# Performance work log

Hardware: AMD Instinct MI355X
Metric: run time of the kernel (lower is better)

## Reference

```python
import jax, jax.numpy as jnp
import numpy as np

N_EMBD = 1024
N_HEAD = 16
MASK_FILL = -10000.0


def setup_inputs() -> dict:
    key = jax.random.key(0)
    ks = jax.random.split(key, 9)
    s = 1.0 / np.sqrt(N_EMBD)
    d = {"x": jax.random.normal(ks[0], (4, 2048, N_EMBD), dtype=jnp.float32)}
    for i, name in enumerate(["k", "q", "v", "p"]):
        d[f"W{name}"] = jax.random.uniform(ks[1 + 2 * i], (N_EMBD, N_EMBD), minval=-s, maxval=s, dtype=jnp.float32)
        d[f"b{name}"] = jax.random.uniform(ks[2 + 2 * i], (N_EMBD,), minval=-s, maxval=s, dtype=jnp.float32)
    return d


def reference(x, Wk, bk, Wq, bq, Wv, bv, Wp, bp):
    B, T, C = x.shape
    H, D = N_HEAD, C // N_HEAD
    # projections -> [B, H, T, D]
    def split_heads(y):
        return y.reshape(B, T, H, D).transpose(0, 2, 1, 3)
    k = split_heads(x @ Wk + bk)
    q = split_heads(x @ Wq + bq)
    v = split_heads(x @ Wv + bv)
    att = jnp.einsum("bhtd,bhsd->bhts", q, k) / jnp.sqrt(jnp.float32(D))
    causal = jnp.tril(jnp.ones((T, T), dtype=bool))  # [T, T]
    att = jnp.where(causal[None, None], att, MASK_FILL)
    att = jax.nn.softmax(att, axis=-1)
    y = jnp.einsum("bhts,bhsd->bhtd", att, v)
    y = y.transpose(0, 2, 1, 3).reshape(B, T, C)
    return y @ Wp + bp
```

## Files before the change

### kernel.cpp

```cpp
#include <hip/hip_runtime.h>
#include <hip/hip_bf16.h>

#define CDIM   1024
#define NHEADS 16
#define DHEAD  64
#define BATCH  4
#define TSEQ   2048
#define MROWS  (BATCH * TSEQ)
#define QSTR   3072
#define NEG_BIG (-1e30f)
#define MASKVAL (-3.0e38f)
#define SCALE_L2E 0.18033688011f
#define DEFER_TH 11.5416f

typedef __attribute__((ext_vector_type(8)))  short bf16x8;
typedef __attribute__((ext_vector_type(4)))  float f32x4;
typedef __attribute__((ext_vector_type(16))) float f32x16;

__device__ __forceinline__ unsigned short f2bf(float f) {
    __hip_bfloat16 h = __float2bfloat16(f);
    return *reinterpret_cast<unsigned short*>(&h);
}
__device__ __forceinline__ unsigned int cvtpk(float a, float b) {
    unsigned r;
    asm("v_cvt_pk_bf16_f32 %0, %1, %2" : "=v"(r) : "v"(a), "v"(b));
    return r;
}
__device__ __forceinline__ float ex2(float x) {
    float r; asm("v_exp_f32 %0, %1" : "=v"(r) : "v"(x)); return r;
}

__global__ __launch_bounds__(256)
void cvt_x_kernel(const float* __restrict__ in, unsigned short* __restrict__ out)
{
    size_t i = (size_t)blockIdx.x * 256 + threadIdx.x;
    const float4* p = reinterpret_cast<const float4*>(in) + i * 2;
    float4 a = p[0], b = p[1];
    uint4 o;
    o.x = (unsigned)f2bf(a.x) | ((unsigned)f2bf(a.y) << 16);
    o.y = (unsigned)f2bf(a.z) | ((unsigned)f2bf(a.w) << 16);
    o.z = (unsigned)f2bf(b.x) | ((unsigned)f2bf(b.y) << 16);
    o.w = (unsigned)f2bf(b.z) | ((unsigned)f2bf(b.w) << 16);
    *reinterpret_cast<uint4*>(out + i * 8) = o;
}

__global__ __launch_bounds__(256)
void wt_kernel(const float* __restrict__ W0, const float* __restrict__ W1,
               const float* __restrict__ W2, const float* __restrict__ W3,
               unsigned short* __restrict__ T0, unsigned short* __restrict__ T1,
               unsigned short* __restrict__ T2, unsigned short* __restrict__ T3)
{
    const float* W; unsigned short* T;
    switch (blockIdx.z) {
        case 0:  W = W0; T = T0; break;
        case 1:  W = W1; T = T1; break;
        case 2:  W = W2; T = T2; break;
        default: W = W3; T = T3; break;
    }
    __shared__ float tile[32][33];
    const int t = threadIdx.x;
    const int r = t >> 3;
    const int c4 = (t & 7) * 4;
    const int n0 = blockIdx.x * 32, k0 = blockIdx.y * 32;
    float4 v = *reinterpret_cast<const float4*>(&W[(size_t)(k0 + r) * CDIM + n0 + c4]);
    tile[r][c4 + 0] = v.x; tile[r][c4 + 1] = v.y;
    tile[r][c4 + 2] = v.z; tile[r][c4 + 3] = v.w;
    __syncthreads();
    uint2 o;
    o.x = (unsigned)f2bf(tile[c4 + 0][r]) | ((unsigned)f2bf(tile[c4 + 1][r]) << 16);
    o.y = (unsigned)f2bf(tile[c4 + 2][r]) | ((unsigned)f2bf(tile[c4 + 3][r]) << 16);
    *reinterpret_cast<uint2*>(&T[(size_t)(n0 + r) * CDIM + k0 + c4]) = o;
}

__global__ __launch_bounds__(256)
void pack_bias(const float* __restrict__ bq, const float* __restrict__ bk,
               const float* __restrict__ bv, float* __restrict__ o)
{
    int i = blockIdx.x * 256 + threadIdx.x;
    float v = (i < 1024) ? bq[i] : (i < 2048 ? bk[i - 1024] : bv[i - 2048]);
    o[i] = v;
}


#define GBAR8  asm volatile("s_barrier" ::: "memory")
#define LGKM0  asm volatile("s_waitcnt lgkmcnt(0)" ::: "memory")
#define VMC4   asm volatile("s_waitcnt vmcnt(4)" ::: "memory")
#define VMC0   asm volatile("s_waitcnt vmcnt(0)" ::: "memory")

#define STAGE8(dsthalf, srcp) do { \
    __builtin_amdgcn_global_load_lds( \
        (const __attribute__((address_space(1))) void*)(srcp), \
        (__attribute__((address_space(3))) void*)((dsthalf) + wv * 1024), 16, 0, 0); \
    __builtin_amdgcn_global_load_lds( \
        (const __attribute__((address_space(1))) void*)((srcp) + 65536), \
        (__attribute__((address_space(3))) void*)((dsthalf) + 8192 + wv * 1024), 16, 0, 0); \
} while (0)

#define LDA8(grp) do { \
    _Pragma("unroll") for (int m_ = 0; m_ < 4; ++m_) { \
        const int rl_ = (grp) * 64 + m_ * 16 + lj; \
        _Pragma("unroll") for (int k_ = 0; k_ < 2; ++k_) \
            af[m_][k_] = *reinterpret_cast<const bf16x8*>( \
                Ab + rl_ * 128 + (((k_ * 4 + lg) ^ (lj & 7)) * 16)); \
    } } while (0)

#define LDB8(pairi) do { \
    _Pragma("unroll") for (int n_ = 0; n_ < 2; ++n_) { \
        const int nr_ = (pairi) * 2 + n_; \
        const int rl_ = (wc & 1) * 64 + nr_ * 16 + lj; \
        _Pragma("unroll") for (int k_ = 0; k_ < 2; ++k_) \
            bfr[nr_][k_] = *reinterpret_cast<const bf16x8*>( \
                Bb + rl_ * 128 + (((k_ * 4 + lg) ^ (lj & 7)) * 16)); \
    } } while (0)

#define MM8(mg, npair) do { \
    __builtin_amdgcn_s_setprio(1); \
    _Pragma("unroll") for (int m_ = 0; m_ < 4; ++m_) \
        _Pragma("unroll") for (int n_ = 0; n_ < 2; ++n_) \
            _Pragma("unroll") for (int k_ = 0; k_ < 2; ++k_) \
                acc[(mg) * 4 + m_][(npair) * 2 + n_] = \
                    __builtin_amdgcn_mfma_f32_16x16x32_bf16( \
                        af[m_][k_], bfr[(npair) * 2 + n_][k_], \
                        acc[(mg) * 4 + m_][(npair) * 2 + n_], 0, 0, 0); \
    __builtin_amdgcn_s_setprio(0); \
} while (0)

__global__ __launch_bounds__(512)
void gemm_8ph(const unsigned short* __restrict__ A,
              const unsigned short* __restrict__ BT,
              const float* __restrict__ bias,
              unsigned short* __restrict__ Cout, int N, int nScaled)
{
    __shared__ __align__(16) char lds8[2][65536];
    const int tid = threadIdx.x;
    const int nbn = N >> 8;
    const int bid = blockIdx.x;
    const int wg  = (bid & 7) * ((int)gridDim.x >> 3) + (bid >> 3);
    const int n0  = (wg % nbn) * 256;
    const int m0  = (wg / nbn) * 256;

    const int lane = tid & 63, wv = tid >> 6;
    const int wr = wv >> 2, wc = wv & 3;
    const int lj = lane & 15, lg = lane >> 4;
    const int srow = tid >> 3;
    const int gsw  = 8 * ((tid & 7) ^ ((tid >> 3) & 7));

    char* buf0 = &lds8[0][0];
    char* buf1 = &lds8[1][0];

    const unsigned short* Alo = A  + (size_t)(m0 + srow) * 1024 + gsw;
    const unsigned short* Ahi = A  + (size_t)(m0 + 128 + srow) * 1024 + gsw;
    const unsigned short* Blo = BT + (size_t)(n0 + srow) * 1024 + gsw;
    const unsigned short* Bhi = BT + (size_t)(n0 + 128 + srow) * 1024 + gsw;

    f32x4 acc[8][4];
    #pragma unroll
    for (int i = 0; i < 8; ++i)
        #pragma unroll
        for (int j = 0; j < 4; ++j) acc[i][j] = f32x4{0.f, 0.f, 0.f, 0.f};

    STAGE8(buf0 + 0,     Alo);
    STAGE8(buf0 + 16384, Ahi);
    STAGE8(buf0 + 32768, Blo);
    STAGE8(buf0 + 49152, Bhi);
    STAGE8(buf1 + 32768, Blo + 64);
    STAGE8(buf1 + 49152, Bhi + 64);
    VMC0; GBAR8;

    bf16x8 af[4][2], bfr[4][2];

    for (int it = 0; it < 8; ++it) {
        const int e = 2 * it, o = e + 1;
        const bool se = (e + 2) < 16;
        const bool so = (o + 2) < 16;

        char* Ab = buf0 + wr * 16384;
        char* Bb = buf0 + 32768 + (wc >> 1) * 16384;
        LDA8(0); LDB8(0);
        STAGE8(buf1 + 0, Alo + o * 64);
        GBAR8; LGKM0; MM8(0, 0); GBAR8;
        LDB8(1);
        STAGE8(buf1 + 16384, Ahi + o * 64);
        GBAR8; LGKM0; MM8(0, 1); GBAR8;
        LDA8(1);
        if (se) STAGE8(buf0 + 32768, Blo + (e + 2) * 64);
        GBAR8; LGKM0; MM8(1, 0); GBAR8;
        if (se) STAGE8(buf0 + 49152, Bhi + (e + 2) * 64);
        GBAR8; LGKM0; MM8(1, 1);
        if (se) { VMC4; } else { VMC0; }
        GBAR8;

        Ab = buf1 + wr * 16384;
        Bb = buf1 + 32768 + (wc >> 1) * 16384;
        LDA8(0); LDB8(0);
        if (se) STAGE8(buf0 + 0, Alo + (e + 2) * 64);
        GBAR8; LGKM0; MM8(0, 0); GBAR8;
        LDB8(1);
        if (se) STAGE8(buf0 + 16384, Ahi + (e + 2) * 64);
        GBAR8; LGKM0; MM8(0, 1); GBAR8;
        LDA8(1);
        if (so) STAGE8(buf1 + 32768, Blo + (o + 2) * 64);
        GBAR8; LGKM0; MM8(1, 0); GBAR8;
        if (so) STAGE8(buf1 + 49152, Bhi + (o + 2) * 64);
        GBAR8; LGKM0; MM8(1, 1);
        if (so) { VMC4; } else { VMC0; }
        GBAR8;
    }

    const float sc = (n0 < nScaled) ? SCALE_L2E : 1.0f;
    float bcol[4];
    #pragma unroll
    for (int nr = 0; nr < 4; ++nr) bcol[nr] = bias[n0 + wc * 64 + nr * 16 + lj];

    #pragma unroll
    for (int mr = 0; mr < 8; ++mr) {
        #pragma unroll
        for (int r4 = 0; r4 < 4; ++r4) {
            const int row = m0 + wr * 128 + mr * 16 + lg * 4 + r4;
            #pragma unroll
            for (int nr = 0; nr < 4; ++nr) {
                const int col = n0 + wc * 64 + nr * 16 + lj;
                Cout[(size_t)row * N + col] = f2bf((acc[mr][nr][r4] + bcol[nr]) * sc);
            }
        }
    }
}

template<int OUTMODE>
__global__ __launch_bounds__(256)
void gemm_glds(const unsigned short* __restrict__ A,
               const unsigned short* __restrict__ BT,
               const float* __restrict__ bias,
               void* __restrict__ Cout, int M, int N, int K, int nScaled)
{
    __shared__ __align__(16) unsigned short As[128 * 64];
    __shared__ __align__(16) unsigned short Bs[128 * 64];
    const int tid = threadIdx.x;
    const int nbn = N >> 7;
    const int bid = blockIdx.x;
    const int wg  = (bid & 7) * ((int)gridDim.x >> 3) + (bid >> 3);
    const int n0  = (wg % nbn) * 128;
    const int m0  = (wg / nbn) * 128;

    const int lane = tid & 63, w = tid >> 6;
    const int wr = w >> 1, wc = w & 1;
    const int lj = lane & 15, lg = lane >> 4;
    const int srow = w * 8 + (lane >> 3);
    const int gsw  = 8 * ((lane & 7) ^ (lane >> 3));

    char* AsB = (char*)As;
    char* BsB = (char*)Bs;

    f32x4 acc[4][4];
    #pragma unroll
    for (int i = 0; i < 4; ++i)
        #pragma unroll
        for (int j = 0; j < 4; ++j) acc[i][j] = f32x4{0.f, 0.f, 0.f, 0.f};

    for (int k0 = 0; k0 < K; k0 += 64) {
        __syncthreads();
        #pragma unroll
        for (int ra = 0; ra < 4; ++ra) {
            const int r = ra * 32 + srow;
            __builtin_amdgcn_global_load_lds(
                (const __attribute__((address_space(1))) void*)(A + (size_t)(m0 + r) * K + k0 + gsw),
                (__attribute__((address_space(3))) void*)(AsB + ra * 4096 + w * 1024),
                16, 0, 0);
            __builtin_amdgcn_global_load_lds(
                (const __attribute__((address_space(1))) void*)(BT + (size_t)(n0 + r) * K + k0 + gsw),
                (__attribute__((address_space(3))) void*)(BsB + ra * 4096 + w * 1024),
                16, 0, 0);
        }
        __syncthreads();
        #pragma unroll
        for (int ks = 0; ks < 2; ++ks) {
            bf16x8 af[4], bfr[4];
            #pragma unroll
            for (int i = 0; i < 4; ++i) {
                const int r = wr * 64 + i * 16 + lj;
                af[i] = *reinterpret_cast<const bf16x8*>(
                    AsB + r * 128 + (((ks * 4 + lg) ^ (lj & 7)) * 16));
            }
            #pragma unroll
            for (int j = 0; j < 4; ++j) {
                const int r = wc * 64 + j * 16 + lj;
                bfr[j] = *reinterpret_cast<const bf16x8*>(
                    BsB + r * 128 + (((ks * 4 + lg) ^ (lj & 7)) * 16));
            }
            #pragma unroll
            for (int i = 0; i < 4; ++i)
                #pragma unroll
                for (int j = 0; j < 4; ++j)
                    acc[i][j] = __builtin_amdgcn_mfma_f32_16x16x32_bf16(af[i], bfr[j], acc[i][j], 0, 0, 0);
        }
    }

    const float sc = (n0 < nScaled) ? SCALE_L2E : 1.0f;
    float bcol[4];
    #pragma unroll
    for (int j = 0; j < 4; ++j) bcol[j] = bias[n0 + wc * 64 + j * 16 + lj];

    #pragma unroll
    for (int i = 0; i < 4; ++i) {
        #pragma unroll
        for (int r4 = 0; r4 < 4; ++r4) {
            const int row = m0 + wr * 64 + i * 16 + lg * 4 + r4;
            #pragma unroll
            for (int j = 0; j < 4; ++j) {
                const int col = n0 + wc * 64 + j * 16 + lj;
                float v = (acc[i][j][r4] + bcol[j]) * sc;
                if (OUTMODE == 0)
                    reinterpret_cast<unsigned short*>(Cout)[(size_t)row * N + col] = f2bf(v);
                else
                    reinterpret_cast<float*>(Cout)[(size_t)row * N + col] = v;
            }
        }
    }
}

#define PV_STEP(m, T, rb) { \
    unsigned int w01 = cvtpk(T[(rb)+0], T[(rb)+1]); \
    unsigned int w23 = cvtpk(T[(rb)+2], T[(rb)+3]); \
    unsigned int w45 = cvtpk(T[(rb)+4], T[(rb)+5]); \
    unsigned int w67 = cvtpk(T[(rb)+6], T[(rb)+7]); \
    asm("v_permlane32_swap_b32 %0, %1" : "+v"(w01), "+v"(w45)); \
    asm("v_permlane32_swap_b32 %0, %1" : "+v"(w23), "+v"(w67)); \
    union { unsigned int u[4]; bf16x8 v; } pa; \
    pa.u[0] = w01; pa.u[1] = w23; pa.u[2] = w45; pa.u[3] = w67; \
    const int voff = (32 * (m) + 16 * hi) ^ lqswz; \
    bf16x8 va = *reinterpret_cast<const bf16x8*>(VTB + lq * 128 + voff); \
    bf16x8 vb = *reinterpret_cast<const bf16x8*>(VTB + (lq + 32) * 128 + voff); \
    y0 = __builtin_amdgcn_mfma_f32_32x32x16_bf16(va, pa.v, y0, 0, 0, 0); \
    y1 = __builtin_amdgcn_mfma_f32_32x32x16_bf16(vb, pa.v, y1, 0, 0, 0); \
}

__global__ __launch_bounds__(256)
void attn_mfma6(const unsigned short* __restrict__ QKV, unsigned short* __restrict__ Yb)
{
    __shared__ unsigned short Ks[64 * 64];
    __shared__ unsigned short VTs[64 * 64];
    __shared__ unsigned short Ysc[4][32 * 72];

    const int tid = threadIdx.x, lane = tid & 63, wid = tid >> 6;
    const int lq = lane & 31, hi = lane >> 5;
    const int lqswz = (lq & 7) << 4;

    const int id  = blockIdx.x;
    const int kk  = id >> 3;
    const int hb  = (id & 7) + 8 * (kk >> 3);
    const int pair = kk & 7;
    const int h = hb & 15, bz = hb >> 4;

    const size_t rowbase = (size_t)bz * TSEQ;
    const int hq = h * DHEAD, hk = 1024 + h * DHEAD, hv = 2048 + h * DHEAD;
    char* KsB = (char*)Ks;
    char* VTB = (char*)VTs;

    const int krow = tid >> 3;
    const int kswz = ((tid & 7) * 16) ^ ((krow & 7) << 4);
    const int vk2  = 2 * (tid & 31);
    const int vdg  = (tid >> 5) * 8;
    const int vkb  = vk2 * 2;

    for (int iter = 0; iter < 2; ++iter) {
        const int qtile = iter ? (15 - pair) : pair;
        const int q0 = qtile * 128;
        const int wq = q0 + wid * 32;

        bf16x8 qf[4];
        {
            const unsigned short* qp = QKV + (rowbase + wq + lq) * QSTR + hq + hi * 8;
            #pragma unroll
            for (int s = 0; s < 4; ++s)
                qf[s] = *reinterpret_cast<const bf16x8*>(qp + s * 16);
        }
        f32x16 y0, y1;
        #pragma unroll
        for (int r = 0; r < 16; ++r) { y0[r] = 0.f; y1[r] = 0.f; }
        float mrow = NEG_BIG, lrow = 0.f;

        const int ktend = 2 * qtile + 2;

        uint4 kr0, kr1, vr0, vr1;
        {
            const unsigned short* kp = QKV + (rowbase + krow) * QSTR + hk + (tid & 7) * 8;
            kr0 = *reinterpret_cast<const uint4*>(kp);
            kr1 = *reinterpret_cast<const uint4*>(kp + 32 * QSTR);
            const unsigned short* vp = QKV + (rowbase + vk2) * QSTR + hv + vdg;
            vr0 = *reinterpret_cast<const uint4*>(vp);
            vr1 = *reinterpret_cast<const uint4*>(vp + QSTR);
        }

        for (int kt = 0; kt < ktend; ++kt) {
            __syncthreads();
            *reinterpret_cast<uint4*>(KsB + krow * 128 + kswz) = kr0;
            *reinterpret_cast<uint4*>(KsB + (krow + 32) * 128 + kswz) = kr1;
            {
                unsigned pe, po;
                pe = __builtin_amdgcn_perm(vr1.x, vr0.x, 0x05040100u);
                po = __builtin_amdgcn_perm(vr1.x, vr0.x, 0x07060302u);
                *reinterpret_cast<unsigned*>(VTB + (vdg + 0) * 128 + (vkb ^ 0x00)) = pe;
                *reinterpret_cast<unsigned*>(VTB + (vdg + 1) * 128 + (vkb ^ 0x10)) = po;
                pe = __builtin_amdgcn_perm(vr1.y, vr0.y, 0x05040100u);
                po = __builtin_amdgcn_perm(vr1.y, vr0.y, 0x07060302u);
                *reinterpret_cast<unsigned*>(VTB + (vdg + 2) * 128 + (vkb ^ 0x20)) = pe;
                *reinterpret_cast<unsigned*>(VTB + (vdg + 3) * 128 + (vkb ^ 0x30)) = po;
                pe = __builtin_amdgcn_perm(vr1.z, vr0.z, 0x05040100u);
                po = __builtin_amdgcn_perm(vr1.z, vr0.z, 0x07060302u);
                *reinterpret_cast<unsigned*>(VTB + (vdg + 4) * 128 + (vkb ^ 0x40)) = pe;
                *reinterpret_cast<unsigned*>(VTB + (vdg + 5) * 128 + (vkb ^ 0x50)) = po;
                pe = __builtin_amdgcn_perm(vr1.w, vr0.w, 0x05040100u);
                po = __builtin_amdgcn_perm(vr1.w, vr0.w, 0x07060302u);
                *reinterpret_cast<unsigned*>(VTB + (vdg + 6) * 128 + (vkb ^ 0x60)) = pe;
                *reinterpret_cast<unsigned*>(VTB + (vdg + 7) * 128 + (vkb ^ 0x70)) = po;
            }
            __syncthreads();

            if (kt + 1 < ktend) {
                const unsigned short* kp = QKV + (rowbase + (kt + 1) * 64 + krow) * QSTR + hk + (tid & 7) * 8;
                kr0 = *reinterpret_cast<const uint4*>(kp);
                kr1 = *reinterpret_cast<const uint4*>(kp + 32 * QSTR);
                const unsigned short* vp = QKV + (rowbase + (kt + 1) * 64 + vk2) * QSTR + hv + vdg;
                vr0 = *reinterpret_cast<const uint4*>(vp);
                vr1 = *reinterpret_cast<const uint4*>(vp + QSTR);
            }

            if (kt * 64 > wq + 31) continue;

            f32x16 s0, s1;
            #pragma unroll
            for (int r = 0; r < 16; ++r) { s0[r] = 0.f; s1[r] = 0.f; }
            #pragma unroll
            for (int s = 0; s < 4; ++s) {
                const int off = (s * 32 + hi * 16) ^ lqswz;
                bf16x8 k0 = *reinterpret_cast<const bf16x8*>(KsB + lq * 128 + off);
                bf16x8 k1 = *reinterpret_cast<const bf16x8*>(KsB + (lq + 32) * 128 + off);
                s0 = __builtin_amdgcn_mfma_f32_32x32x16_bf16(k0, qf[s], s0, 0, 0, 0);
                s1 = __builtin_amdgcn_mfma_f32_32x32x16_bf16(k1, qf[s], s1, 0, 0, 0);
            }

            const bool diag = (kt * 64 + 63) > wq;
            if (diag) {
                const int q_own = wq + lq;
                #pragma unroll
                for (int r = 0; r < 16; ++r) {
                    const int kl = kt * 64 + (r & 3) + 8 * (r >> 2) + 4 * hi;
                    if (kl > q_own) s0[r] = MASKVAL;
                    if (kl + 32 > q_own) s1[r] = MASKVAL;
                }
            }

            float t8[8];
            #pragma unroll
            for (int r = 0; r < 8; ++r)
                t8[r] = fmaxf(fmaxf(s0[r], s0[r + 8]), fmaxf(s1[r], s1[r + 8]));
            #pragma unroll
            for (int r = 0; r < 4; ++r) t8[r] = fmaxf(t8[r], t8[r + 4]);
            float pm = fmaxf(fmaxf(t8[0], t8[1]), fmaxf(t8[2], t8[3]));
            pm = fmaxf(pm, __shfl_xor(pm, 32));

            if (__any(pm > mrow + DEFER_TH)) {
                const float mnew = fmaxf(mrow, pm);
                const float alpha = ex2(mrow - mnew);
                #pragma unroll
                for (int r = 0; r < 16; ++r) { y0[r] *= alpha; y1[r] *= alpha; }
                lrow *= alpha;
                mrow = mnew;
            }
            #pragma unroll
            for (int r = 0; r < 16; ++r) {
                s0[r] = ex2(s0[r] - mrow);
                s1[r] = ex2(s1[r] - mrow);
            }
            float a8[8];
            #pragma unroll
            for (int r = 0; r < 8; ++r) a8[r] = (s0[r] + s0[r + 8]) + (s1[r] + s1[r + 8]);
            #pragma unroll
            for (int r = 0; r < 4; ++r) a8[r] += a8[r + 4];
            float sum = (a8[0] + a8[1]) + (a8[2] + a8[3]);
            sum += __shfl_xor(sum, 32);
            lrow += sum;

            PV_STEP(0, s0, 0)
            PV_STEP(1, s0, 8)
            PV_STEP(2, s1, 0)
            PV_STEP(3, s1, 8)
        }

        {
            const float inv = 1.f / lrow;
            char* ysb = (char*)&Ysc[wid][0];
            #pragma unroll
            for (int t = 0; t < 8; ++t) {
                const int dl = ((2 * t) & 3) + 8 * (t >> 1) + 4 * hi;
                unsigned int wa = cvtpk(y0[2 * t] * inv, y0[2 * t + 1] * inv);
                unsigned int wb = cvtpk(y1[2 * t] * inv, y1[2 * t + 1] * inv);
                *reinterpret_cast<unsigned int*>(ysb + lq * 144 + dl * 2) = wa;
                *reinterpret_cast<unsigned int*>(ysb + lq * 144 + (dl + 32) * 2) = wb;
            }
            #pragma unroll
            for (int u = 0; u < 4; ++u) {
                const int rr = lane >> 1, ch = (lane & 1) + 2 * u;
                uint4 val = *reinterpret_cast<const uint4*>(ysb + rr * 144 + ch * 16);
                *reinterpret_cast<uint4*>(Yb + (rowbase + q0 + wid * 32 + rr) * CDIM + h * DHEAD + ch * 8) = val;
            }
        }
    }
}

extern "C" void kernel_launch(void* const* d_in, const int* in_sizes, int n_in,
                              void* d_out, int out_size, void* d_ws, size_t ws_size,
                              hipStream_t stream)
{
    const float* x  = (const float*)d_in[0];
    const float* Wk = (const float*)d_in[1];
    const float* bk = (const float*)d_in[2];
    const float* Wq = (const float*)d_in[3];
    const float* bq = (const float*)d_in[4];
    const float* Wv = (const float*)d_in[5];
    const float* bv = (const float*)d_in[6];
    const float* Wp = (const float*)d_in[7];
    const float* bp = (const float*)d_in[8];

    const size_t xe = (size_t)MROWS * CDIM;
    const size_t we = (size_t)CDIM * CDIM;
    unsigned short* xb    = (unsigned short*)d_ws;
    unsigned short* wqkvt = xb + xe;
    unsigned short* wpt   = wqkvt + 3 * we;
    unsigned short* qkv   = wpt + we;
    unsigned short* ab    = qkv + (size_t)MROWS * QSTR;
    float*          bias3 = (float*)(ab + xe);

    cvt_x_kernel<<<(int)(xe / 8 / 256), 256, 0, stream>>>(x, xb);
    wt_kernel<<<dim3(32, 32, 4), 256, 0, stream>>>(
        Wq, Wk, Wv, Wp, wqkvt, wqkvt + we, wqkvt + 2 * we, wpt);
    pack_bias<<<12, 256, 0, stream>>>(bq, bk, bv, bias3);

    gemm_8ph<<<32 * 12, 512, 0, stream>>>(xb, wqkvt, bias3, qkv, QSTR, 1024);

    attn_mfma6<<<512, 256, 0, stream>>>(qkv, ab);

    gemm_glds<1><<<8 * 64, 256, 0, stream>>>(ab, wpt, bp, d_out,
                                             MROWS, CDIM, CDIM, 0);
}
```

Measured before the change: 169.0 us.

## Split attention into one query tile per block with balanced tile ordering

The attention kernel no longer has each block process a pair of query tiles (short plus long) in a loop. It now launches 1024 blocks, each handling a single 128-row query tile, and orders tiles across four waves of the grid so that long and short causal tiles interleave. This exposes twice as many blocks to fill the 256 CUs and aims to cut tail imbalance. In exchange, per-block work becomes uneven, so the result depends on how the hardware schedules blocks.

Result: no change. 170.1 us (+0.6%).

```diff
diff --git a/kernel.cpp b/kernel.cpp
--- a/kernel.cpp
+++ b/kernel.cpp
@@ -80,7 +80,6 @@
     float v = (i < 1024) ? bq[i] : (i < 2048 ? bk[i - 1024] : bv[i - 2048]);
     o[i] = v;
 }
-
 
 #define GBAR8  asm volatile("s_barrier" ::: "memory")
 #define LGKM0  asm volatile("s_waitcnt lgkmcnt(0)" ::: "memory")
@@ -335,7 +334,7 @@
 }
 
 __global__ __launch_bounds__(256)
-void attn_mfma6(const unsigned short* __restrict__ QKV, unsigned short* __restrict__ Yb)
+void attn_mfma8(const unsigned short* __restrict__ QKV, unsigned short* __restrict__ Yb)
 {
     __shared__ unsigned short Ks[64 * 64];
     __shared__ unsigned short VTs[64 * 64];
@@ -345,11 +344,16 @@
     const int lq = lane & 31, hi = lane >> 5;
     const int lqswz = (lq & 7) << 4;
 
-    const int id  = blockIdx.x;
-    const int kk  = id >> 3;
-    const int hb  = (id & 7) + 8 * (kk >> 3);
-    const int pair = kk & 7;
-    const int h = hb & 15, bz = hb >> 4;
+    const int id = blockIdx.x;
+    const int x  = id & 7;
+    const int u  = id >> 3;
+    const int k  = u >> 5;
+    const int s  = u & 31;
+    const int y  = s & 7;
+    const int t  = s >> 3;
+    const int hb = x + 8 * y;
+    const int h  = hb & 15, bz = hb >> 4;
+    const int qtile = (k == 0) ? t : (k == 1) ? (15 - t) : (k == 2) ? (t + 4) : (11 - t);
 
     const size_t rowbase = (size_t)bz * TSEQ;
     const int hq = h * DHEAD, hk = 1024 + h * DHEAD, hv = 2048 + h * DHEAD;
@@ -362,148 +366,145 @@
     const int vdg  = (tid >> 5) * 8;
     const int vkb  = vk2 * 2;
 
-    for (int iter = 0; iter < 2; ++iter) {
-        const int qtile = iter ? (15 - pair) : pair;
-        const int q0 = qtile * 128;
-        const int wq = q0 + wid * 32;
-
-        bf16x8 qf[4];
+    const int q0 = qtile * 128;
+    const int wq = q0 + wid * 32;
+
+    bf16x8 qf[4];
+    {
+        const unsigned short* qp = QKV + (rowbase + wq + lq) * QSTR + hq + hi * 8;
+        #pragma unroll
+        for (int ss = 0; ss < 4; ++ss)
+            qf[ss] = *reinterpret_cast<const bf16x8*>(qp + ss * 16);
+    }
+    f32x16 y0, y1;
+    #pragma unroll
+    for (int r = 0; r < 16; ++r) { y0[r] = 0.f; y1[r] = 0.f; }
+    float mrow = NEG_BIG, lrow = 0.f;
+
+    const int ktend = 2 * qtile + 2;
+
+    uint4 kr0, kr1, vr0, vr1;
+    {
+        const unsigned short* kp = QKV + (rowbase + krow) * QSTR + hk + (tid & 7) * 8;
+        kr0 = *reinterpret_cast<const uint4*>(kp);
+        kr1 = *reinterpret_cast<const uint4*>(kp + 32 * QSTR);
+        const unsigned short* vp = QKV + (rowbase + vk2) * QSTR + hv + vdg;
+        vr0 = *reinterpret_cast<const uint4*>(vp);
+        vr1 = *reinterpret_cast<const uint4*>(vp + QSTR);
+    }
+
+    for (int kt = 0; kt < ktend; ++kt) {
+        __syncthreads();
+        *reinterpret_cast<uint4*>(KsB + krow * 128 + kswz) = kr0;
+        *reinterpret_cast<uint4*>(KsB + (krow + 32) * 128 + kswz) = kr1;
         {
-            const unsigned short* qp = QKV + (rowbase + wq + lq) * QSTR + hq + hi * 8;
-            #pragma unroll
-            for (int s = 0; s < 4; ++s)
-                qf[s] = *reinterpret_cast<const bf16x8*>(qp + s * 16);
-        }
-        f32x16 y0, y1;
-        #pragma unroll
-        for (int r = 0; r < 16; ++r) { y0[r] = 0.f; y1[r] = 0.f; }
-        float mrow = NEG_BIG, lrow = 0.f;
-
-        const int ktend = 2 * qtile + 2;
-
-        uint4 kr0, kr1, vr0, vr1;
-        {
-            const unsigned short* kp = QKV + (rowbase + krow) * QSTR + hk + (tid & 7) * 8;
+            unsigned pe, po;
+            pe = __builtin_amdgcn_perm(vr1.x, vr0.x, 0x05040100u);
+            po = __builtin_amdgcn_perm(vr1.x, vr0.x, 0x07060302u);
+            *reinterpret_cast<unsigned*>(VTB + (vdg + 0) * 128 + (vkb ^ 0x00)) = pe;
+            *reinterpret_cast<unsigned*>(VTB + (vdg + 1) * 128 + (vkb ^ 0x10)) = po;
+            pe = __builtin_amdgcn_perm(vr1.y, vr0.y, 0x05040100u);
+            po = __builtin_amdgcn_perm(vr1.y, vr0.y, 0x07060302u);
+            *reinterpret_cast<unsigned*>(VTB + (vdg + 2) * 128 + (vkb ^ 0x20)) = pe;
+            *reinterpret_cast<unsigned*>(VTB + (vdg + 3) * 128 + (vkb ^ 0x30)) = po;
+            pe = __builtin_amdgcn_perm(vr1.z, vr0.z, 0x05040100u);
+            po = __builtin_amdgcn_perm(vr1.z, vr0.z, 0x07060302u);
+            *reinterpret_cast<unsigned*>(VTB + (vdg + 4) * 128 + (vkb ^ 0x40)) = pe;
+            *reinterpret_cast<unsigned*>(VTB + (vdg + 5) * 128 + (vkb ^ 0x50)) = po;
+            pe = __builtin_amdgcn_perm(vr1.w, vr0.w, 0x05040100u);
+            po = __builtin_amdgcn_perm(vr1.w, vr0.w, 0x07060302u);
+            *reinterpret_cast<unsigned*>(VTB + (vdg + 6) * 128 + (vkb ^ 0x60)) = pe;
+            *reinterpret_cast<unsigned*>(VTB + (vdg + 7) * 128 + (vkb ^ 0x70)) = po;
+        }
+        __syncthreads();
+
+        if (kt + 1 < ktend) {
+            const unsigned short* kp = QKV + (rowbase + (kt + 1) * 64 + krow) * QSTR + hk + (tid & 7) * 8;
             kr0 = *reinterpret_cast<const uint4*>(kp);
             kr1 = *reinterpret_cast<const uint4*>(kp + 32 * QSTR);
-            const unsigned short* vp = QKV + (rowbase + vk2) * QSTR + hv + vdg;
+            const unsigned short* vp = QKV + (rowbase + (kt + 1) * 64 + vk2) * QSTR + hv + vdg;
             vr0 = *reinterpret_cast<const uint4*>(vp);
             vr1 = *reinterpret_cast<const uint4*>(vp + QSTR);
         }
 
-        for (int kt = 0; kt < ktend; ++kt) {
-            __syncthreads();
-            *reinterpret_cast<uint4*>(KsB + krow * 128 + kswz) = kr0;
-            *reinterpret_cast<uint4*>(KsB + (krow + 32) * 128 + kswz) = kr1;
-            {
-                unsigned pe, po;
-                pe = __builtin_amdgcn_perm(vr1.x, vr0.x, 0x05040100u);
-                po = __builtin_amdgcn_perm(vr1.x, vr0.x, 0x07060302u);
-                *reinterpret_cast<unsigned*>(VTB + (vdg + 0) * 128 + (vkb ^ 0x00)) = pe;
-                *reinterpret_cast<unsigned*>(VTB + (vdg + 1) * 128 + (vkb ^ 0x10)) = po;
-                pe = __builtin_amdgcn_perm(vr1.y, vr0.y, 0x05040100u);
-                po = __builtin_amdgcn_perm(vr1.y, vr0.y, 0x07060302u);
-                *reinterpret_cast<unsigned*>(VTB + (vdg + 2) * 128 + (vkb ^ 0x20)) = pe;
-                *reinterpret_cast<unsigned*>(VTB + (vdg + 3) * 128 + (vkb ^ 0x30)) = po;
-                pe = __builtin_amdgcn_perm(vr1.z, vr0.z, 0x05040100u);
-                po = __builtin_amdgcn_perm(vr1.z, vr0.z, 0x07060302u);
-                *reinterpret_cast<unsigned*>(VTB + (vdg + 4) * 128 + (vkb ^ 0x40)) = pe;
-                *reinterpret_cast<unsigned*>(VTB + (vdg + 5) * 128 + (vkb ^ 0x50)) = po;
-                pe = __builtin_amdgcn_perm(vr1.w, vr0.w, 0x05040100u);
-                po = __builtin_amdgcn_perm(vr1.w, vr0.w, 0x07060302u);
-                *reinterpret_cast<unsigned*>(VTB + (vdg + 6) * 128 + (vkb ^ 0x60)) = pe;
-                *reinterpret_cast<unsigned*>(VTB + (vdg + 7) * 128 + (vkb ^ 0x70)) = po;
+        if (kt * 64 > wq + 31) continue;
+
+        f32x16 s0, s1;
+        #pragma unroll
+        for (int r = 0; r < 16; ++r) { s0[r] = 0.f; s1[r] = 0.f; }
+        #pragma unroll
+        for (int ss = 0; ss < 4; ++ss) {
+            const int off = (ss * 32 + hi * 16) ^ lqswz;
+            bf16x8 k0 = *reinterpret_cast<const bf16x8*>(KsB + lq * 128 + off);
+            bf16x8 k1 = *reinterpret_cast<const bf16x8*>(KsB + (lq + 32) * 128 + off);
+            s0 = __builtin_amdgcn_mfma_f32_32x32x16_bf16(k0, qf[ss], s0, 0, 0, 0);
+            s1 = __builtin_amdgcn_mfma_f32_32x32x16_bf16(k1, qf[ss], s1, 0, 0, 0);
+        }
+
+        const bool diag = (kt * 64 + 63) > wq;
+        if (diag) {
+            const int q_own = wq + lq;
+            #pragma unroll
+            for (int r = 0; r < 16; ++r) {
+                const int kl = kt * 64 + (r & 3) + 8 * (r >> 2) + 4 * hi;
+                if (kl > q_own) s0[r] = MASKVAL;
+                if (kl + 32 > q_own) s1[r] = MASKVAL;
             }
-            __syncthreads();
-
-            if (kt + 1 < ktend) {
-                const unsigned short* kp = QKV + (rowbase + (kt + 1) * 64 + krow) * QSTR + hk + (tid & 7) * 8;
-                kr0 = *reinterpret_cast<const uint4*>(kp);
-                kr1 = *reinterpret_cast<const uint4*>(kp + 32 * QSTR);
-                const unsigned short* vp = QKV + (rowbase + (kt + 1) * 64 + vk2) * QSTR + hv + vdg;
-                vr0 = *reinterpret_cast<const uint4*>(vp);
-                vr1 = *reinterpret_cast<const uint4*>(vp + QSTR);
-            }
-
-            if (kt * 64 > wq + 31) continue;
-
-            f32x16 s0, s1;
-            #pragma unroll
-            for (int r = 0; r < 16; ++r) { s0[r] = 0.f; s1[r] = 0.f; }
-            #pragma unroll
-            for (int s = 0; s < 4; ++s) {
-                const int off = (s * 32 + hi * 16) ^ lqswz;
-                bf16x8 k0 = *reinterpret_cast<const bf16x8*>(KsB + lq * 128 + off);
-                bf16x8 k1 = *reinterpret_cast<const bf16x8*>(KsB + (lq + 32) * 128 + off);
-                s0 = __builtin_amdgcn_mfma_f32_32x32x16_bf16(k0, qf[s], s0, 0, 0, 0);
-                s1 = __builtin_amdgcn_mfma_f32_32x32x16_bf16(k1, qf[s], s1, 0, 0, 0);
-            }
-
-            const bool diag = (kt * 64 + 63) > wq;
-            if (diag) {
-                const int q_own = wq + lq;
-                #pragma unroll
-                for (int r = 0; r < 16; ++r) {
-                    const int kl = kt * 64 + (r & 3) + 8 * (r >> 2) + 4 * hi;
-                    if (kl > q_own) s0[r] = MASKVAL;
-                    if (kl + 32 > q_own) s1[r] = MASKVAL;
-                }
-            }
-
-            float t8[8];
-            #pragma unroll
-            for (int r = 0; r < 8; ++r)
-                t8[r] = fmaxf(fmaxf(s0[r], s0[r + 8]), fmaxf(s1[r], s1[r + 8]));
-            #pragma unroll
-            for (int r = 0; r < 4; ++r) t8[r] = fmaxf(t8[r], t8[r + 4]);
-            float pm = fmaxf(fmaxf(t8[0], t8[1]), fmaxf(t8[2], t8[3]));
-            pm = fmaxf(pm, __shfl_xor(pm, 32));
-
-            if (__any(pm > mrow + DEFER_TH)) {
-                const float mnew = fmaxf(mrow, pm);
-                const float alpha = ex2(mrow - mnew);
-                #pragma unroll
-                for (int r = 0; r < 16; ++r) { y0[r] *= alpha; y1[r] *= alpha; }
-                lrow *= alpha;
-                mrow = mnew;
-            }
-            #pragma unroll
-            for (int r = 0; r < 16; ++r) {
-                s0[r] = ex2(s0[r] - mrow);
-                s1[r] = ex2(s1[r] - mrow);
-            }
-            float a8[8];
-            #pragma unroll
-            for (int r = 0; r < 8; ++r) a8[r] = (s0[r] + s0[r + 8]) + (s1[r] + s1[r + 8]);
-            #pragma unroll
-            for (int r = 0; r < 4; ++r) a8[r] += a8[r + 4];
-            float sum = (a8[0] + a8[1]) + (a8[2] + a8[3]);
-            sum += __shfl_xor(sum, 32);
-            lrow += sum;
-
-            PV_STEP(0, s0, 0)
-            PV_STEP(1, s0, 8)
-            PV_STEP(2, s1, 0)
-            PV_STEP(3, s1, 8)
-        }
-
-        {
-            const float inv = 1.f / lrow;
-            char* ysb = (char*)&Ysc[wid][0];
-            #pragma unroll
-            for (int t = 0; t < 8; ++t) {
-                const int dl = ((2 * t) & 3) + 8 * (t >> 1) + 4 * hi;
-                unsigned int wa = cvtpk(y0[2 * t] * inv, y0[2 * t + 1] * inv);
-                unsigned int wb = cvtpk(y1[2 * t] * inv, y1[2 * t + 1] * inv);
-                *reinterpret_cast<unsigned int*>(ysb + lq * 144 + dl * 2) = wa;
-                *reinterpret_cast<unsigned int*>(ysb + lq * 144 + (dl + 32) * 2) = wb;
-            }
-            #pragma unroll
-            for (int u = 0; u < 4; ++u) {
-                const int rr = lane >> 1, ch = (lane & 1) + 2 * u;
-                uint4 val = *reinterpret_cast<const uint4*>(ysb + rr * 144 + ch * 16);
-                *reinterpret_cast<uint4*>(Yb + (rowbase + q0 + wid * 32 + rr) * CDIM + h * DHEAD + ch * 8) = val;
-            }
+        }
+
+        float t8[8];
+        #pragma unroll
+        for (int r = 0; r < 8; ++r)
+            t8[r] = fmaxf(fmaxf(s0[r], s0[r + 8]), fmaxf(s1[r], s1[r + 8]));
+        #pragma unroll
+        for (int r = 0; r < 4; ++r) t8[r] = fmaxf(t8[r], t8[r + 4]);
+        float pm = fmaxf(fmaxf(t8[0], t8[1]), fmaxf(t8[2], t8[3]));
+        pm = fmaxf(pm, __shfl_xor(pm, 32));
+
+        if (__any(pm > mrow + DEFER_TH)) {
+            const float mnew = fmaxf(mrow, pm);
+            const float alpha = ex2(mrow - mnew);
+            #pragma unroll
+            for (int r = 0; r < 16; ++r) { y0[r] *= alpha; y1[r] *= alpha; }
+            lrow *= alpha;
+            mrow = mnew;
+        }
+        #pragma unroll
+        for (int r = 0; r < 16; ++r) {
+            s0[r] = ex2(s0[r] - mrow);
+            s1[r] = ex2(s1[r] - mrow);
+        }
+        float a8[8];
+        #pragma unroll
+        for (int r = 0; r < 8; ++r) a8[r] = (s0[r] + s0[r + 8]) + (s1[r] + s1[r + 8]);
+        #pragma unroll
+        for (int r = 0; r < 4; ++r) a8[r] += a8[r + 4];
+        float sum = (a8[0] + a8[1]) + (a8[2] + a8[3]);
+        sum += __shfl_xor(sum, 32);
+        lrow += sum;
+
+        PV_STEP(0, s0, 0)
+        PV_STEP(1, s0, 8)
+        PV_STEP(2, s1, 0)
+        PV_STEP(3, s1, 8)
+    }
+
+    {
+        const float inv = 1.f / lrow;
+        char* ysb = (char*)&Ysc[wid][0];
+        #pragma unroll
+        for (int tt = 0; tt < 8; ++tt) {
+            const int dl = ((2 * tt) & 3) + 8 * (tt >> 1) + 4 * hi;
+            unsigned int wa = cvtpk(y0[2 * tt] * inv, y0[2 * tt + 1] * inv);
+            unsigned int wb = cvtpk(y1[2 * tt] * inv, y1[2 * tt + 1] * inv);
+            *reinterpret_cast<unsigned int*>(ysb + lq * 144 + dl * 2) = wa;
+            *reinterpret_cast<unsigned int*>(ysb + lq * 144 + (dl + 32) * 2) = wb;
+        }
+        #pragma unroll
+        for (int uu = 0; uu < 4; ++uu) {
+            const int rr = lane >> 1, ch = (lane & 1) + 2 * uu;
+            uint4 val = *reinterpret_cast<const uint4*>(ysb + rr * 144 + ch * 16);
+            *reinterpret_cast<uint4*>(Yb + (rowbase + q0 + wid * 32 + rr) * CDIM + h * DHEAD + ch * 8) = val;
         }
     }
 }
@@ -538,7 +539,7 @@
 
     gemm_8ph<<<32 * 12, 512, 0, stream>>>(xb, wqkvt, bias3, qkv, QSTR, 1024);
 
-    attn_mfma6<<<512, 256, 0, stream>>>(qkv, ab);
+    attn_mfma8<<<1024, 256, 0, stream>>>(qkv, ab);
 
     gemm_glds<1><<<8 * 64, 256, 0, stream>>>(ab, wpt, bp, d_out,
                                              MROWS, CDIM, CDIM, 0);
```

## Enlarge attention key/value tile from 64 to 128 keys per iteration

Applied to the files above, without the earlier changes.

The attention kernel now stages 128 keys of K and V into shared memory per loop iteration instead of 64. Each iteration issues four score MFMAs and eight PV MFMAs, which halves the number of iterations and block-wide barriers and gives the MFMA units more independent work between syncs. In exchange it raises register and LDS use, which may lower occupancy. It also does more masked wasted work on the diagonal tile. The V transpose is rewritten to pack bf16 pairs element by element rather than with the byte-permute instruction, into a 256-byte row-stride swizzled layout.

New measurement: 216.3 us. +28.0%, slower.

```diff
diff --git a/kernel.cpp b/kernel.cpp
--- a/kernel.cpp
+++ b/kernel.cpp
@@ -81,7 +81,6 @@
     o[i] = v;
 }
 
-
 #define GBAR8  asm volatile("s_barrier" ::: "memory")
 #define LGKM0  asm volatile("s_waitcnt lgkmcnt(0)" ::: "memory")
 #define VMC4   asm volatile("s_waitcnt vmcnt(4)" ::: "memory")
@@ -318,7 +317,7 @@
     }
 }
 
-#define PV_STEP(m, T, rb) { \
+#define PV_STEP9(m, T, rb) { \
     unsigned int w01 = cvtpk(T[(rb)+0], T[(rb)+1]); \
     unsigned int w23 = cvtpk(T[(rb)+2], T[(rb)+3]); \
     unsigned int w45 = cvtpk(T[(rb)+4], T[(rb)+5]); \
@@ -328,17 +327,17 @@
     union { unsigned int u[4]; bf16x8 v; } pa; \
     pa.u[0] = w01; pa.u[1] = w23; pa.u[2] = w45; pa.u[3] = w67; \
     const int voff = (32 * (m) + 16 * hi) ^ lqswz; \
-    bf16x8 va = *reinterpret_cast<const bf16x8*>(VTB + lq * 128 + voff); \
-    bf16x8 vb = *reinterpret_cast<const bf16x8*>(VTB + (lq + 32) * 128 + voff); \
+    bf16x8 va = *reinterpret_cast<const bf16x8*>(VTB + lq * 256 + voff); \
+    bf16x8 vb = *reinterpret_cast<const bf16x8*>(VTB + (lq + 32) * 256 + voff); \
     y0 = __builtin_amdgcn_mfma_f32_32x32x16_bf16(va, pa.v, y0, 0, 0, 0); \
     y1 = __builtin_amdgcn_mfma_f32_32x32x16_bf16(vb, pa.v, y1, 0, 0, 0); \
 }
 
 __global__ __launch_bounds__(256)
-void attn_mfma6(const unsigned short* __restrict__ QKV, unsigned short* __restrict__ Yb)
-{
-    __shared__ unsigned short Ks[64 * 64];
-    __shared__ unsigned short VTs[64 * 64];
+void attn_mfma9(const unsigned short* __restrict__ QKV, unsigned short* __restrict__ Yb)
+{
+    __shared__ unsigned short Ks[128 * 64];
+    __shared__ unsigned short VTs[64 * 128];
     __shared__ unsigned short Ysc[4][32 * 72];
 
     const int tid = threadIdx.x, lane = tid & 63, wid = tid >> 6;
@@ -356,11 +355,12 @@
     char* KsB = (char*)Ks;
     char* VTB = (char*)VTs;
 
-    const int krow = tid >> 3;
-    const int kswz = ((tid & 7) * 16) ^ ((krow & 7) << 4);
-    const int vk2  = 2 * (tid & 31);
-    const int vdg  = (tid >> 5) * 8;
-    const int vkb  = vk2 * 2;
+    const int krow  = tid >> 3;
+    const int kcol8 = (tid & 7) * 8;
+    const int kswz  = ((tid & 7) * 16) ^ ((krow & 7) << 4);
+    const int vk2   = 2 * (tid & 63);
+    const int vdg   = (tid >> 6) * 8;
+    const int vkb   = vk2 * 2;
 
     for (int iter = 0; iter < 2; ++iter) {
         const int qtile = iter ? (15 - pair) : pair;
@@ -379,81 +379,91 @@
         for (int r = 0; r < 16; ++r) { y0[r] = 0.f; y1[r] = 0.f; }
         float mrow = NEG_BIG, lrow = 0.f;
 
-        const int ktend = 2 * qtile + 2;
-
-        uint4 kr0, kr1, vr0, vr1;
+        const int ktend = qtile + 1;
+
+        uint4 kr[4], vr[4];
         {
-            const unsigned short* kp = QKV + (rowbase + krow) * QSTR + hk + (tid & 7) * 8;
-            kr0 = *reinterpret_cast<const uint4*>(kp);
-            kr1 = *reinterpret_cast<const uint4*>(kp + 32 * QSTR);
+            const unsigned short* kp = QKV + (rowbase + krow) * QSTR + hk + kcol8;
+            #pragma unroll
+            for (int p = 0; p < 4; ++p)
+                kr[p] = *reinterpret_cast<const uint4*>(kp + 32 * p * QSTR);
             const unsigned short* vp = QKV + (rowbase + vk2) * QSTR + hv + vdg;
-            vr0 = *reinterpret_cast<const uint4*>(vp);
-            vr1 = *reinterpret_cast<const uint4*>(vp + QSTR);
+            vr[0] = *reinterpret_cast<const uint4*>(vp);
+            vr[1] = *reinterpret_cast<const uint4*>(vp + QSTR);
+            vr[2] = *reinterpret_cast<const uint4*>(vp + 32);
+            vr[3] = *reinterpret_cast<const uint4*>(vp + QSTR + 32);
         }
 
         for (int kt = 0; kt < ktend; ++kt) {
             __syncthreads();
-            *reinterpret_cast<uint4*>(KsB + krow * 128 + kswz) = kr0;
-            *reinterpret_cast<uint4*>(KsB + (krow + 32) * 128 + kswz) = kr1;
-            {
-                unsigned pe, po;
-                pe = __builtin_amdgcn_perm(vr1.x, vr0.x, 0x05040100u);
-                po = __builtin_amdgcn_perm(vr1.x, vr0.x, 0x07060302u);
-                *reinterpret_cast<unsigned*>(VTB + (vdg + 0) * 128 + (vkb ^ 0x00)) = pe;
-                *reinterpret_cast<unsigned*>(VTB + (vdg + 1) * 128 + (vkb ^ 0x10)) = po;
-                pe = __builtin_amdgcn_perm(vr1.y, vr0.y, 0x05040100u);
-                po = __builtin_amdgcn_perm(vr1.y, vr0.y, 0x07060302u);
-                *reinterpret_cast<unsigned*>(VTB + (vdg + 2) * 128 + (vkb ^ 0x20)) = pe;
-                *reinterpret_cast<unsigned*>(VTB + (vdg + 3) * 128 + (vkb ^ 0x30)) = po;
-                pe = __builtin_amdgcn_perm(vr1.z, vr0.z, 0x05040100u);
-                po = __builtin_amdgcn_perm(vr1.z, vr0.z, 0x07060302u);
-                *reinterpret_cast<unsigned*>(VTB + (vdg + 4) * 128 + (vkb ^ 0x40)) = pe;
-                *reinterpret_cast<unsigned*>(VTB + (vdg + 5) * 128 + (vkb ^ 0x50)) = po;
-                pe = __builtin_amdgcn_perm(vr1.w, vr0.w, 0x05040100u);
-                po = __builtin_amdgcn_perm(vr1.w, vr0.w, 0x07060302u);
-                *reinterpret_cast<unsigned*>(VTB + (vdg + 6) * 128 + (vkb ^ 0x60)) = pe;
-                *reinterpret_cast<unsigned*>(VTB + (vdg + 7) * 128 + (vkb ^ 0x70)) = po;
+            #pragma unroll
+            for (int p = 0; p < 4; ++p)
+                *reinterpret_cast<uint4*>(KsB + (krow + 32 * p) * 128 + kswz) = kr[p];
+            #pragma unroll
+            for (int half = 0; half < 2; ++half) {
+                unsigned short a8[8], b8[8];
+                *reinterpret_cast<uint4*>(a8) = vr[2 * half];
+                *reinterpret_cast<uint4*>(b8) = vr[2 * half + 1];
+                const int dbase = vdg + 32 * half;
+                #pragma unroll
+                for (int i2 = 0; i2 < 8; ++i2) {
+                    unsigned int w = (unsigned)a8[i2] | ((unsigned)b8[i2] << 16);
+                    const int d = dbase + i2;
+                    *reinterpret_cast<unsigned*>(VTB + d * 256 + (vkb ^ ((d & 7) << 4))) = w;
+                }
             }
             __syncthreads();
 
             if (kt + 1 < ktend) {
-                const unsigned short* kp = QKV + (rowbase + (kt + 1) * 64 + krow) * QSTR + hk + (tid & 7) * 8;
-                kr0 = *reinterpret_cast<const uint4*>(kp);
-                kr1 = *reinterpret_cast<const uint4*>(kp + 32 * QSTR);
-                const unsigned short* vp = QKV + (rowbase + (kt + 1) * 64 + vk2) * QSTR + hv + vdg;
-                vr0 = *reinterpret_cast<const uint4*>(vp);
-                vr1 = *reinterpret_cast<const uint4*>(vp + QSTR);
-            }
-
-            if (kt * 64 > wq + 31) continue;
-
-            f32x16 s0, s1;
-            #pragma unroll
-            for (int r = 0; r < 16; ++r) { s0[r] = 0.f; s1[r] = 0.f; }
-            #pragma unroll
-            for (int s = 0; s < 4; ++s) {
-                const int off = (s * 32 + hi * 16) ^ lqswz;
+                const unsigned short* kp = QKV + (rowbase + (kt + 1) * 128 + krow) * QSTR + hk + kcol8;
+                #pragma unroll
+                for (int p = 0; p < 4; ++p)
+                    kr[p] = *reinterpret_cast<const uint4*>(kp + 32 * p * QSTR);
+                const unsigned short* vp = QKV + (rowbase + (kt + 1) * 128 + vk2) * QSTR + hv + vdg;
+                vr[0] = *reinterpret_cast<const uint4*>(vp);
+                vr[1] = *reinterpret_cast<const uint4*>(vp + QSTR);
+                vr[2] = *reinterpret_cast<const uint4*>(vp + 32);
+                vr[3] = *reinterpret_cast<const uint4*>(vp + QSTR + 32);
+            }
+
+            if (kt * 128 > wq + 31) continue;
+
+            f32x16 s0, s1, s2, s3;
+            #pragma unroll
+            for (int r = 0; r < 16; ++r) { s0[r] = 0.f; s1[r] = 0.f; s2[r] = 0.f; s3[r] = 0.f; }
+            #pragma unroll
+            for (int ss = 0; ss < 4; ++ss) {
+                const int off = (ss * 32 + hi * 16) ^ lqswz;
                 bf16x8 k0 = *reinterpret_cast<const bf16x8*>(KsB + lq * 128 + off);
                 bf16x8 k1 = *reinterpret_cast<const bf16x8*>(KsB + (lq + 32) * 128 + off);
-                s0 = __builtin_amdgcn_mfma_f32_32x32x16_bf16(k0, qf[s], s0, 0, 0, 0);
-                s1 = __builtin_amdgcn_mfma_f32_32x32x16_bf16(k1, qf[s], s1, 0, 0, 0);
-            }
-
-            const bool diag = (kt * 64 + 63) > wq;
+                bf16x8 k2 = *reinterpret_cast<const bf16x8*>(KsB + (lq + 64) * 128 + off);
+                bf16x8 k3 = *reinterpret_cast<const bf16x8*>(KsB + (lq + 96) * 128 + off);
+                s0 = __builtin_amdgcn_mfma_f32_32x32x16_bf16(k0, qf[ss], s0, 0, 0, 0);
+                s1 = __builtin_amdgcn_mfma_f32_32x32x16_bf16(k1, qf[ss], s1, 0, 0, 0);
+                s2 = __builtin_amdgcn_mfma_f32_32x32x16_bf16(k2, qf[ss], s2, 0, 0, 0);
+                s3 = __builtin_amdgcn_mfma_f32_32x32x16_bf16(k3, qf[ss], s3, 0, 0, 0);
+            }
+
+            const bool diag = (kt * 128 + 127) > wq;
             if (diag) {
                 const int q_own = wq + lq;
                 #pragma unroll
                 for (int r = 0; r < 16; ++r) {
-                    const int kl = kt * 64 + (r & 3) + 8 * (r >> 2) + 4 * hi;
-                    if (kl > q_own) s0[r] = MASKVAL;
+                    const int kl = kt * 128 + (r & 3) + 8 * (r >> 2) + 4 * hi;
+                    if (kl      > q_own) s0[r] = MASKVAL;
                     if (kl + 32 > q_own) s1[r] = MASKVAL;
+                    if (kl + 64 > q_own) s2[r] = MASKVAL;
+                    if (kl + 96 > q_own) s3[r] = MASKVAL;
                 }
             }
 
             float t8[8];
             #pragma unroll
-            for (int r = 0; r < 8; ++r)
-                t8[r] = fmaxf(fmaxf(s0[r], s0[r + 8]), fmaxf(s1[r], s1[r + 8]));
+            for (int r = 0; r < 8; ++r) {
+                float a = fmaxf(fmaxf(s0[r], s0[r + 8]), fmaxf(s1[r], s1[r + 8]));
+                float b = fmaxf(fmaxf(s2[r], s2[r + 8]), fmaxf(s3[r], s3[r + 8]));
+                t8[r] = fmaxf(a, b);
+            }
             #pragma unroll
             for (int r = 0; r < 4; ++r) t8[r] = fmaxf(t8[r], t8[r + 4]);
             float pm = fmaxf(fmaxf(t8[0], t8[1]), fmaxf(t8[2], t8[3]));
@@ -471,20 +481,28 @@
             for (int r = 0; r < 16; ++r) {
                 s0[r] = ex2(s0[r] - mrow);
                 s1[r] = ex2(s1[r] - mrow);
+                s2[r] = ex2(s2[r] - mrow);
+                s3[r] = ex2(s3[r] - mrow);
             }
             float a8[8];
             #pragma unroll
-            for (int r = 0; r < 8; ++r) a8[r] = (s0[r] + s0[r + 8]) + (s1[r] + s1[r + 8]);
+            for (int r = 0; r < 8; ++r)
+                a8[r] = ((s0[r] + s0[r + 8]) + (s1[r] + s1[r + 8]))
+                      + ((s2[r] + s2[r + 8]) + (s3[r] + s3[r + 8]));
             #pragma unroll
             for (int r = 0; r < 4; ++r) a8[r] += a8[r + 4];
             float sum = (a8[0] + a8[1]) + (a8[2] + a8[3]);
             sum += __shfl_xor(sum, 32);
             lrow += sum;
 
-            PV_STEP(0, s0, 0)
-            PV_STEP(1, s0, 8)
-            PV_STEP(2, s1, 0)
-            PV_STEP(3, s1, 8)
+            PV_STEP9(0, s0, 0)
+            PV_STEP9(1, s0, 8)
+            PV_STEP9(2, s1, 0)
+            PV_STEP9(3, s1, 8)
+            PV_STEP9(4, s2, 0)
+            PV_STEP9(5, s2, 8)
+            PV_STEP9(6, s3, 0)
+            PV_STEP9(7, s3, 8)
         }
 
         {
@@ -538,7 +556,7 @@
 
     gemm_8ph<<<32 * 12, 512, 0, stream>>>(xb, wqkvt, bias3, qkv, QSTR, 1024);
 
-    attn_mfma6<<<512, 256, 0, stream>>>(qkv, ab);
+    attn_mfma9<<<512, 256, 0, stream>>>(qkv, ab);
 
     gemm_glds<1><<<8 * 64, 256, 0, stream>>>(ab, wpt, bp, d_out,
                                              MROWS, CDIM, CDIM, 0);
```
